# Performance work log

Hardware: AMD Instinct MI355X
Metric: run time of the kernel (lower is better)

The kernel has to match this reference:

```python
import jax, jax.numpy as jnp
import numpy as np

L_COMPUTE = 32   # topological levels after primary inputs
W = 32768        # gates per level
K = 4            # max fan-in (distinct pins 1..K per gate)
B = 128          # parallel test patterns
T = 16           # number of cell types in the library
N = (L_COMPUTE + 1) * W


def setup_inputs() -> dict:
    key = jax.random.key(0)
    k1, k2, k3, k4 = jax.random.split(key, 4)
    # binary logic values per node per pattern (only level-0 rows are real inputs;
    # the rest are overwritten by propagation, matching g.ndata['h'] = feature)
    feature = jax.random.bernoulli(k1, 0.5, (N, B)).astype(jnp.float32)
    # truth table: activation[cell_type, input_combination] in {0,1}
    activation = jax.random.bernoulli(k2, 0.5, (T, 2 ** K)).astype(jnp.float32)
    # each gate in level l draws its K inputs from level l-1
    src_idx = jax.random.randint(k3, (L_COMPUTE, W, K), 0, W).astype(jnp.int32)
    cell_type = jax.random.randint(k4, (L_COMPUTE, W), 0, T).astype(jnp.int32)
    # edge pin numbers: distinct pins 1..K per gate (edges.data['x'])
    pins = jnp.broadcast_to(jnp.arange(1, K + 1, dtype=jnp.int32), (L_COMPUTE, W, K))
    pins = jnp.asarray(pins)
    return {"feature": feature, "activation": activation, "src_idx": src_idx,
            "cell_type": cell_type, "pins": pins}


def reference(feature, activation, src_idx, cell_type, pins):
    Wn = src_idx.shape[1]
    Bn = feature.shape[1]
    h0 = feature[:Wn]  # primary-input level keeps its feature values

    def step(h, xs):
        src, ctype, pin = xs          # [W,K], [W], [W,K]
        hs = h[src]                   # gather: [W,K,B]
        # gcn_msg: m = 2^(x-1) * h_src ; gcn_reduce: sum over incoming edges
        w = jnp.exp2(pin.astype(h.dtype) - 1.0)          # [W,K]
        m = jnp.einsum('wk,wkb->wb', w, hs)              # [W,B] encoded input combo
        # NodeApplyModule: truth-table lookup activation[cell_type, h]
        h_new = activation[ctype[:, None], m.astype(jnp.int32)]  # [W,B]
        return h_new, h_new

    _, ys = jax.lax.scan(step, h0, (src_idx, cell_type, pins))
    # g.ndata.pop('h'): values for ALL nodes, level 0 unchanged
    return jnp.concatenate([h0, ys.reshape(-1, Bn)], axis=0)
```

## Files before the change

### kernel.cpp

```cpp
#include <hip/hip_runtime.h>
#include <stdint.h>

typedef uint32_t u32;
typedef unsigned long long u64;
typedef float f4 __attribute__((ext_vector_type(4)));

#define WGATES 32768
#define BATCH  128
#define LAYERS 32
#define NTYPES 16
#define NC 128
#define WPL (WGATES * 4)
#define F4L (WGATES * BATCH / 4)

#define WS_SUB_OFF    1024
#define WS_LVL2_OFF   34816
#define WS_DONE_OFF   35840
#define WS_S_OFF      69632
#define WS_NEED_BYTES ((size_t)(WS_S_OFF + 33 * WPL) * 4)

__device__ __forceinline__ u32 agent_load(const u32* p) {
    return __hip_atomic_load(p, __ATOMIC_RELAXED, __HIP_MEMORY_SCOPE_AGENT);
}
__device__ __forceinline__ void agent_store(u32* p, u32 v) {
    __hip_atomic_store(p, v, __ATOMIC_RELAXED, __HIP_MEMORY_SCOPE_AGENT);
}
__device__ __forceinline__ void agent_store64(u64* p, u64 v) {
    __hip_atomic_store(p, v, __ATOMIC_RELAXED, __HIP_MEMORY_SCOPE_AGENT);
}
__device__ __forceinline__ u32 agent_add(u32* p, u32 v) {
    return __hip_atomic_fetch_add(p, v, __ATOMIC_RELAXED, __HIP_MEMORY_SCOPE_AGENT);
}

__device__ __forceinline__ void lut_masks(u32 tt, u32 m[16]) {
    #pragma unroll
    for (int j = 0; j < 16; ++j)
        m[j] = (u32)(((int)(tt << (31 - j))) >> 31);
}
__device__ __forceinline__ u32 lut_mux(const u32 m[16], u32 a, u32 b, u32 c, u32 d) {
    u32 na = ~a, nb = ~b, nc = ~c, nd = ~d;
    u32 v0 = (m[1]&a)|(m[0]&na),  v1 = (m[3]&a)|(m[2]&na);
    u32 v2 = (m[5]&a)|(m[4]&na),  v3 = (m[7]&a)|(m[6]&na);
    u32 v4 = (m[9]&a)|(m[8]&na),  v5 = (m[11]&a)|(m[10]&na);
    u32 v6 = (m[13]&a)|(m[12]&na),v7 = (m[15]&a)|(m[14]&na);
    u32 u0 = (b&v1)|(nb&v0), u1 = (b&v3)|(nb&v2);
    u32 u2 = (b&v5)|(nb&v4), u3 = (b&v7)|(nb&v6);
    u32 w0 = (c&u1)|(nc&u0), w1 = (c&u3)|(nc&u2);
    return (d&w1)|(nd&w0);
}

__device__ __forceinline__ void wait_done(const u32* ws, int l, int line,
                                          int tid, int slp) {
    if (tid == 0) {
        const u32* p = ws + WS_DONE_OFF + (size_t)l * 1024 + line * 16;
        if (slp == 1) { while (agent_load(p) == 0) __builtin_amdgcn_s_sleep(1); }
        else         { while (agent_load(p) == 0) __builtin_amdgcn_s_sleep(8); }
    }
    __syncthreads();
    asm volatile("" ::: "memory");
}

__global__ void pack_main(const float* __restrict__ feature,
                          const float* __restrict__ activation,
                          u32* __restrict__ ws) {
    int t = blockIdx.x * 256 + threadIdx.x;
    if (blockIdx.x == 0 && threadIdx.x < NTYPES) {
        u32 tt = 0;
        #pragma unroll
        for (int m = 0; m < 16; ++m)
            tt |= (activation[threadIdx.x * 16 + m] != 0.0f ? 1u : 0u) << m;
        ws[threadIdx.x] = tt;
    }
    int z = (int)blockIdx.x - 1;
    if (z >= 0 && z < 268)
        ws[1024 + z * 256 + threadIdx.x] = 0;
    float v = feature[t];
    u64 m = __ballot(v != 0.0f);
    if ((t & 63) == 0)
        ((u64*)(ws + WS_S_OFF))[t >> 6] = m;
}

__global__ __launch_bounds__(256) void coop_kernel(
        const int* __restrict__ src_idx,
        const int* __restrict__ cell_type,
        u32* __restrict__ ws,
        float* __restrict__ out,
        int NU)
{
    u32* Sb = ws + WS_S_OFF;
    int tid = threadIdx.x;
    __shared__ u32 stt[NTYPES];
    if (tid < NTYPES) stt[tid] = ws[tid];
    __syncthreads();

    if ((int)blockIdx.x < NC) {
        int g = blockIdx.x * 256 + tid;
        int sub = blockIdx.x & 15;
        for (int l = 1; l <= LAYERS; ++l) {
            const int4 s = ((const int4*)(src_idx + (size_t)(l - 1) * WGATES * 4))[g];
            u32 ttv = stt[cell_type[(size_t)(l - 1) * WGATES + g]];
            if (l > 1) wait_done(ws, l - 1, sub, tid, 1);
            const uint4* Sp = (const uint4*)(Sb + (size_t)(l - 1) * WPL);
            uint4 A = Sp[(u32)s.x];
            uint4 B = Sp[(u32)s.y];
            uint4 C = Sp[(u32)s.z];
            uint4 D = Sp[(u32)s.w];
            u32 m[16];
            lut_masks(ttv, m);
            u32 r0 = lut_mux(m, A.x, B.x, C.x, D.x);
            u32 r1 = lut_mux(m, A.y, B.y, C.y, D.y);
            u32 r2 = lut_mux(m, A.z, B.z, C.z, D.z);
            u32 r3 = lut_mux(m, A.w, B.w, C.w, D.w);
            u64* dst = (u64*)(Sb + (size_t)l * WPL + (size_t)g * 4);
            agent_store64(dst,     ((u64)r1 << 32) | r0);
            agent_store64(dst + 1, ((u64)r3 << 32) | r2);
            asm volatile("s_waitcnt vmcnt(0)" ::: "memory");
            __syncthreads();
            if (tid == 0) {
                u32* subp = ws + WS_SUB_OFF + (size_t)l * 1024 + sub * 16;
                u32 old = agent_add(subp, 1u);
                if (old == (u32)(NC / 16 - 1)) {
                    u32 old2 = agent_add(ws + WS_LVL2_OFF + (size_t)l * 16, 1u);
                    if (old2 == 15u) {
                        u32* donep = ws + WS_DONE_OFF + (size_t)l * 1024;
                        #pragma unroll
                        for (int j = 0; j < 64; ++j)
                            agent_store(donep + j * 16, 1u);
                    }
                }
            }
        }
    } else {
        int ub = blockIdx.x - NC;
        bool sliced = (NU & 7) == 0;
        int x = ub & 7;
        u32 per = (u32)(NU >> 3);
        for (int l = 0; l <= LAYERS; ++l) {
            if (l >= 1) wait_done(ws, l, ub & 63, tid, 8);
            const u32* Sl = Sb + (size_t)l * WPL;
            f4* ob = (f4*)(out + (size_t)l * WGATES * BATCH);
            if (sliced) {
                u32 sbeg = (u32)x * (F4L / 8), send = sbeg + F4L / 8;
                for (u32 i = sbeg + (u32)(ub >> 3) * 256u + tid; i < send;
                     i += per * 256u) {
                    u32 wb = Sl[i >> 3];
                    u32 sh = (i & 7) * 4;
                    f4 f;
                    f.x = ((wb >> (sh    )) & 1) ? 1.0f : 0.0f;
                    f.y = ((wb >> (sh + 1)) & 1) ? 1.0f : 0.0f;
                    f.z = ((wb >> (sh + 2)) & 1) ? 1.0f : 0.0f;
                    f.w = ((wb >> (sh + 3)) & 1) ? 1.0f : 0.0f;
                    __builtin_nontemporal_store(f, ob + i);
                }
            } else {
                for (u32 i = (u32)ub * 256u + tid; i < (u32)F4L;
                     i += (u32)NU * 256u) {
                    u32 wb = Sl[i >> 3];
                    u32 sh = (i & 7) * 4;
                    f4 f;
                    f.x = ((wb >> (sh    )) & 1) ? 1.0f : 0.0f;
                    f.y = ((wb >> (sh + 1)) & 1) ? 1.0f : 0.0f;
                    f.z = ((wb >> (sh + 2)) & 1) ? 1.0f : 0.0f;
                    f.w = ((wb >> (sh + 3)) & 1) ? 1.0f : 0.0f;
                    __builtin_nontemporal_store(f, ob + i);
                }
            }
        }
    }
}

__global__ void pack_kernel_fb(const float* __restrict__ feature,
                               const float* __restrict__ activation,
                               float* __restrict__ out,
                               u32* __restrict__ tt_ws,
                               u32* __restrict__ buf0) {
    int t = blockIdx.x * 256 + threadIdx.x;
    if (blockIdx.x == 0 && threadIdx.x < NTYPES) {
        u32 tt = 0;
        #pragma unroll
        for (int m = 0; m < 16; ++m)
            tt |= (activation[threadIdx.x * 16 + m] != 0.0f ? 1u : 0u) << m;
        tt_ws[threadIdx.x] = tt;
    }
    float v = feature[t];
    out[t] = v;
    u64 m = __ballot(v != 0.0f);
    if ((t & 63) == 0)
        ((u64*)buf0)[t >> 6] = m;
}

__global__ void fused_kernel_fb(const u32* __restrict__ prev,
                                u32* __restrict__ next,
                                const int* __restrict__ src_idx,
                                const int* __restrict__ cell_type,
                                const u32* __restrict__ tt_ws,
                                const u32* __restrict__ upacked,
                                float* __restrict__ uout,
                                int do_compute)
{
    int tid = threadIdx.x;
    if (do_compute && blockIdx.x < 512) {
        int gl = tid >> 2, q = tid & 3;
        int wg = blockIdx.x * 64 + gl;
        const int4 s = ((const int4*)src_idx)[wg];
        u32 tt = tt_ws[cell_type[wg]];
        u32 m[16];
        lut_masks(tt, m);
        u32 a = prev[(size_t)s.x * 4 + q];
        u32 b = prev[(size_t)s.y * 4 + q];
        u32 c = prev[(size_t)s.z * 4 + q];
        u32 d = prev[(size_t)s.w * 4 + q];
        next[(size_t)wg * 4 + q] = lut_mux(m, a, b, c, d);
        return;
    }
    if (uout == nullptr) return;
    int ub = do_compute ? (int)blockIdx.x - 512 : (int)blockIdx.x;
    #pragma unroll
    for (int r = 0; r < 2; ++r) {
        int fi = ((ub * 2 + r) * 256 + tid) * 4;
        u32 wb = upacked[fi >> 5];
        int sh = fi & 31;
        f4 f;
        f.x = ((wb >> (sh    )) & 1) ? 1.0f : 0.0f;
        f.y = ((wb >> (sh + 1)) & 1) ? 1.0f : 0.0f;
        f.z = ((wb >> (sh + 2)) & 1) ? 1.0f : 0.0f;
        f.w = ((wb >> (sh + 3)) & 1) ? 1.0f : 0.0f;
        ((f4*)uout)[fi >> 2] = f;
    }
}

static void launch_fallback(const float* feature, const float* activation,
                            const int* src_idx, const int* cell_type,
                            float* out, void* d_ws, hipStream_t stream) {
    u32* tt_ws = (u32*)d_ws;
    u32* bufA = (u32*)((char*)d_ws + 1024);
    u32* bufB = (u32*)((char*)d_ws + 1024 + WGATES * 16);
    pack_kernel_fb<<<WGATES * BATCH / 256, 256, 0, stream>>>(
        feature, activation, out, tt_ws, bufA);
    for (int l = 1; l <= LAYERS; ++l) {
        u32* prev = ((l - 1) & 1) ? bufB : bufA;
        u32* next = ((l - 1) & 1) ? bufA : bufB;
        float* uout = (l >= 2) ? out + (size_t)(l - 1) * WGATES * BATCH : nullptr;
        fused_kernel_fb<<<512 + 2048, 256, 0, stream>>>(
            prev, next,
            src_idx + (size_t)(l - 1) * WGATES * 4,
            cell_type + (size_t)(l - 1) * WGATES,
            tt_ws, prev, uout, 1);
    }
    u32* s32 = ((LAYERS - 1) & 1) ? bufA : bufB;
    fused_kernel_fb<<<2048, 256, 0, stream>>>(
        s32, s32, src_idx, cell_type, tt_ws,
        s32, out + (size_t)LAYERS * WGATES * BATCH, 0);
}

extern "C" void kernel_launch(void* const* d_in, const int* in_sizes, int n_in,
                              void* d_out, int out_size, void* d_ws, size_t ws_size,
                              hipStream_t stream) {
    const float* feature    = (const float*)d_in[0];
    const float* activation = (const float*)d_in[1];
    const int*   src_idx    = (const int*)d_in[2];
    const int*   cell_type  = (const int*)d_in[3];
    float* out = (float*)d_out;

    bool coop_ok = (ws_size >= WS_NEED_BYTES);
    int G = 0, NU = 0;
    if (coop_ok) {
        int dev = 0;
        (void)hipGetDevice(&dev);
        int numCU = 0, bpc = 0;
        if (hipDeviceGetAttribute(&numCU, hipDeviceAttributeMultiprocessorCount, dev)
                != hipSuccess) coop_ok = false;
        if (coop_ok &&
            hipOccupancyMaxActiveBlocksPerMultiprocessor(
                &bpc, (const void*)coop_kernel, 256, 0) != hipSuccess) coop_ok = false;
        if (coop_ok) {
            G = bpc * numCU;
            if (G > 2048) G = 2048;
            NU = G - NC;
            if (NU < 256) coop_ok = false;
        }
    }

    if (coop_ok) {
        u32* ws = (u32*)d_ws;
        pack_main<<<WGATES * BATCH / 256, 256, 0, stream>>>(feature, activation, ws);
        void* args[] = {(void*)&src_idx, (void*)&cell_type, (void*)&ws,
                        (void*)&out, (void*)&NU};
        hipError_t e = hipLaunchCooperativeKernel(
            (const void*)coop_kernel, dim3(G), dim3(256), args, 0, stream);
        if (e == hipSuccess) return;
    }
    launch_fallback(feature, activation, src_idx, cell_type, out, d_ws, stream);
}
```

Before: 166.6 us.

## Compute two levels per grid barrier by recomputing level-1 fan-in gates redundantly

Each compute block now handles two topological levels per barrier round. For the second level it recomputes its four first-level input gates directly from the level l-2 state, so grid-wide barriers drop from 32 to 16. The price is about 5x more gathers and LUT evaluations per round and a larger register footprint. The writer blocks now wait per round and emit two levels at a time.

```diff
diff --git a/kernel.cpp b/kernel.cpp
--- a/kernel.cpp
+++ b/kernel.cpp
@@ -8,6 +8,7 @@
 #define WGATES 32768
 #define BATCH  128
 #define LAYERS 32
+#define NROUND (LAYERS / 2)
 #define NTYPES 16
 #define NC 128
 #define WPL (WGATES * 4)
@@ -49,10 +50,10 @@
     return (d&w1)|(nd&w0);
 }
 
-__device__ __forceinline__ void wait_done(const u32* ws, int l, int line,
+__device__ __forceinline__ void wait_done(const u32* ws, int r, int line,
                                           int tid, int slp) {
     if (tid == 0) {
-        const u32* p = ws + WS_DONE_OFF + (size_t)l * 1024 + line * 16;
+        const u32* p = ws + WS_DONE_OFF + (size_t)r * 1024 + line * 16;
         if (slp == 1) { while (agent_load(p) == 0) __builtin_amdgcn_s_sleep(1); }
         else         { while (agent_load(p) == 0) __builtin_amdgcn_s_sleep(8); }
     }
@@ -96,33 +97,75 @@
     if ((int)blockIdx.x < NC) {
         int g = blockIdx.x * 256 + tid;
         int sub = blockIdx.x & 15;
-        for (int l = 1; l <= LAYERS; ++l) {
-            const int4 s = ((const int4*)(src_idx + (size_t)(l - 1) * WGATES * 4))[g];
-            u32 ttv = stt[cell_type[(size_t)(l - 1) * WGATES + g]];
-            if (l > 1) wait_done(ws, l - 1, sub, tid, 1);
-            const uint4* Sp = (const uint4*)(Sb + (size_t)(l - 1) * WPL);
-            uint4 A = Sp[(u32)s.x];
-            uint4 B = Sp[(u32)s.y];
-            uint4 C = Sp[(u32)s.z];
-            uint4 D = Sp[(u32)s.w];
+        for (int r = 1; r <= NROUND; ++r) {
+            const int l1 = 2 * r - 1, l2 = 2 * r;
+            const int4* S1 = (const int4*)(src_idx + (size_t)(l1 - 1) * WGATES * 4);
+            const int4* S2 = (const int4*)(src_idx + (size_t)(l2 - 1) * WGATES * 4);
+            const int*  C1 = cell_type + (size_t)(l1 - 1) * WGATES;
+            const int*  C2 = cell_type + (size_t)(l2 - 1) * WGATES;
+            int4 i1 = S1[g];
+            int4 i2 = S2[g];
+            u32 c1 = stt[C1[g]];
+            u32 c2 = stt[C2[g]];
+            int4 j0 = S1[(u32)i2.x];  u32 cj0 = stt[C1[i2.x]];
+            int4 j1 = S1[(u32)i2.y];  u32 cj1 = stt[C1[i2.y]];
+            int4 j2 = S1[(u32)i2.z];  u32 cj2 = stt[C1[i2.z]];
+            int4 j3 = S1[(u32)i2.w];  u32 cj3 = stt[C1[i2.w]];
+
+            if (r > 1) wait_done(ws, r - 1, sub, tid, 1);
+
+            const uint4* Sp = (const uint4*)(Sb + (size_t)(2 * r - 2) * WPL);
+            uint4 A  = Sp[(u32)i1.x], B  = Sp[(u32)i1.y],
+                  C  = Sp[(u32)i1.z], D  = Sp[(u32)i1.w];
+            uint4 A0 = Sp[(u32)j0.x], B0 = Sp[(u32)j0.y],
+                  C0 = Sp[(u32)j0.z], D0 = Sp[(u32)j0.w];
+            uint4 A1 = Sp[(u32)j1.x], B1 = Sp[(u32)j1.y],
+                  C1v= Sp[(u32)j1.z], D1 = Sp[(u32)j1.w];
+            uint4 A2 = Sp[(u32)j2.x], B2 = Sp[(u32)j2.y],
+                  C2v= Sp[(u32)j2.z], D2 = Sp[(u32)j2.w];
+            uint4 A3 = Sp[(u32)j3.x], B3 = Sp[(u32)j3.y],
+                  C3 = Sp[(u32)j3.z], D3 = Sp[(u32)j3.w];
+
             u32 m[16];
-            lut_masks(ttv, m);
-            u32 r0 = lut_mux(m, A.x, B.x, C.x, D.x);
-            u32 r1 = lut_mux(m, A.y, B.y, C.y, D.y);
-            u32 r2 = lut_mux(m, A.z, B.z, C.z, D.z);
-            u32 r3 = lut_mux(m, A.w, B.w, C.w, D.w);
-            u64* dst = (u64*)(Sb + (size_t)l * WPL + (size_t)g * 4);
-            agent_store64(dst,     ((u64)r1 << 32) | r0);
-            agent_store64(dst + 1, ((u64)r3 << 32) | r2);
+            lut_masks(c1, m);
+            u32 o0 = lut_mux(m, A.x, B.x, C.x, D.x);
+            u32 o1 = lut_mux(m, A.y, B.y, C.y, D.y);
+            u32 o2 = lut_mux(m, A.z, B.z, C.z, D.z);
+            u32 o3 = lut_mux(m, A.w, B.w, C.w, D.w);
+            u64* d1 = (u64*)(Sb + (size_t)l1 * WPL + (size_t)g * 4);
+            agent_store64(d1,     ((u64)o1 << 32) | o0);
+            agent_store64(d1 + 1, ((u64)o3 << 32) | o2);
+            uint4 s0, s1v, s2v, s3v;
+            lut_masks(cj0, m);
+            s0.x = lut_mux(m, A0.x,B0.x,C0.x,D0.x); s0.y = lut_mux(m, A0.y,B0.y,C0.y,D0.y);
+            s0.z = lut_mux(m, A0.z,B0.z,C0.z,D0.z); s0.w = lut_mux(m, A0.w,B0.w,C0.w,D0.w);
+            lut_masks(cj1, m);
+            s1v.x = lut_mux(m, A1.x,B1.x,C1v.x,D1.x); s1v.y = lut_mux(m, A1.y,B1.y,C1v.y,D1.y);
+            s1v.z = lut_mux(m, A1.z,B1.z,C1v.z,D1.z); s1v.w = lut_mux(m, A1.w,B1.w,C1v.w,D1.w);
+            lut_masks(cj2, m);
+            s2v.x = lut_mux(m, A2.x,B2.x,C2v.x,D2.x); s2v.y = lut_mux(m, A2.y,B2.y,C2v.y,D2.y);
+            s2v.z = lut_mux(m, A2.z,B2.z,C2v.z,D2.z); s2v.w = lut_mux(m, A2.w,B2.w,C2v.w,D2.w);
+            lut_masks(cj3, m);
+            s3v.x = lut_mux(m, A3.x,B3.x,C3.x,D3.x); s3v.y = lut_mux(m, A3.y,B3.y,C3.y,D3.y);
+            s3v.z = lut_mux(m, A3.z,B3.z,C3.z,D3.z); s3v.w = lut_mux(m, A3.w,B3.w,C3.w,D3.w);
+            lut_masks(c2, m);
+            u32 e0 = lut_mux(m, s0.x, s1v.x, s2v.x, s3v.x);
+            u32 e1 = lut_mux(m, s0.y, s1v.y, s2v.y, s3v.y);
+            u32 e2 = lut_mux(m, s0.z, s1v.z, s2v.z, s3v.z);
+            u32 e3 = lut_mux(m, s0.w, s1v.w, s2v.w, s3v.w);
+            u64* d2 = (u64*)(Sb + (size_t)l2 * WPL + (size_t)g * 4);
+            agent_store64(d2,     ((u64)e1 << 32) | e0);
+            agent_store64(d2 + 1, ((u64)e3 << 32) | e2);
+
             asm volatile("s_waitcnt vmcnt(0)" ::: "memory");
             __syncthreads();
             if (tid == 0) {
-                u32* subp = ws + WS_SUB_OFF + (size_t)l * 1024 + sub * 16;
+                u32* subp = ws + WS_SUB_OFF + (size_t)r * 1024 + sub * 16;
                 u32 old = agent_add(subp, 1u);
                 if (old == (u32)(NC / 16 - 1)) {
-                    u32 old2 = agent_add(ws + WS_LVL2_OFF + (size_t)l * 16, 1u);
+                    u32 old2 = agent_add(ws + WS_LVL2_OFF + (size_t)r * 16, 1u);
                     if (old2 == 15u) {
-                        u32* donep = ws + WS_DONE_OFF + (size_t)l * 1024;
+                        u32* donep = ws + WS_DONE_OFF + (size_t)r * 1024;
                         #pragma unroll
                         for (int j = 0; j < 64; ++j)
                             agent_store(donep + j * 16, 1u);
@@ -135,34 +178,38 @@
         bool sliced = (NU & 7) == 0;
         int x = ub & 7;
         u32 per = (u32)(NU >> 3);
-        for (int l = 0; l <= LAYERS; ++l) {
-            if (l >= 1) wait_done(ws, l, ub & 63, tid, 8);
-            const u32* Sl = Sb + (size_t)l * WPL;
-            f4* ob = (f4*)(out + (size_t)l * WGATES * BATCH);
-            if (sliced) {
-                u32 sbeg = (u32)x * (F4L / 8), send = sbeg + F4L / 8;
-                for (u32 i = sbeg + (u32)(ub >> 3) * 256u + tid; i < send;
-                     i += per * 256u) {
-                    u32 wb = Sl[i >> 3];
-                    u32 sh = (i & 7) * 4;
-                    f4 f;
-                    f.x = ((wb >> (sh    )) & 1) ? 1.0f : 0.0f;
-                    f.y = ((wb >> (sh + 1)) & 1) ? 1.0f : 0.0f;
-                    f.z = ((wb >> (sh + 2)) & 1) ? 1.0f : 0.0f;
-                    f.w = ((wb >> (sh + 3)) & 1) ? 1.0f : 0.0f;
-                    __builtin_nontemporal_store(f, ob + i);
-                }
-            } else {
-                for (u32 i = (u32)ub * 256u + tid; i < (u32)F4L;
-                     i += (u32)NU * 256u) {
-                    u32 wb = Sl[i >> 3];
-                    u32 sh = (i & 7) * 4;
-                    f4 f;
-                    f.x = ((wb >> (sh    )) & 1) ? 1.0f : 0.0f;
-                    f.y = ((wb >> (sh + 1)) & 1) ? 1.0f : 0.0f;
-                    f.z = ((wb >> (sh + 2)) & 1) ? 1.0f : 0.0f;
-                    f.w = ((wb >> (sh + 3)) & 1) ? 1.0f : 0.0f;
-                    __builtin_nontemporal_store(f, ob + i);
+        for (int r = 0; r <= NROUND; ++r) {
+            if (r >= 1) wait_done(ws, r, ub & 63, tid, 8);
+            int lbeg = (r == 0) ? 0 : 2 * r - 1;
+            int lend = (r == 0) ? 0 : 2 * r;
+            for (int l = lbeg; l <= lend; ++l) {
+                const u32* Sl = Sb + (size_t)l * WPL;
+                f4* ob = (f4*)(out + (size_t)l * WGATES * BATCH);
+                if (sliced) {
+                    u32 sbeg = (u32)x * (F4L / 8), send = sbeg + F4L / 8;
+                    for (u32 i = sbeg + (u32)(ub >> 3) * 256u + tid; i < send;
+                         i += per * 256u) {
+                        u32 wb = Sl[i >> 3];
+                        u32 sh = (i & 7) * 4;
+                        f4 f;
+                        f.x = ((wb >> (sh    )) & 1) ? 1.0f : 0.0f;
+                        f.y = ((wb >> (sh + 1)) & 1) ? 1.0f : 0.0f;
+                        f.z = ((wb >> (sh + 2)) & 1) ? 1.0f : 0.0f;
+                        f.w = ((wb >> (sh + 3)) & 1) ? 1.0f : 0.0f;
+                        __builtin_nontemporal_store(f, ob + i);
+                    }
+                } else {
+                    for (u32 i = (u32)ub * 256u + tid; i < (u32)F4L;
+                         i += (u32)NU * 256u) {
+                        u32 wb = Sl[i >> 3];
+                        u32 sh = (i & 7) * 4;
+                        f4 f;
+                        f.x = ((wb >> (sh    )) & 1) ? 1.0f : 0.0f;
+                        f.y = ((wb >> (sh + 1)) & 1) ? 1.0f : 0.0f;
+                        f.z = ((wb >> (sh + 2)) & 1) ? 1.0f : 0.0f;
+                        f.w = ((wb >> (sh + 3)) & 1) ? 1.0f : 0.0f;
+                        __builtin_nontemporal_store(f, ob + i);
+                    }
                 }
             }
         }
```

Result: slower. 249.5 us (+49.8%).

## Replace per-level barrier with epoch-tagged words for dataflow synchronization

Applied to the files above, without the earlier changes.

Adds a coop_epoch kernel that stores each packed 32-bit word next to a 32-bit level tag. Compute blocks now gather their inputs optimistically and spin only on entries whose tag is stale, instead of waiting on a full level barrier. The barrier signal is deferred and used only by the unpacking blocks, and next-level indices are prefetched early. This doubles the workspace footprint and the gather bytes, and it relies on relaxed 64-bit atomic visibility. The path is selected only when the workspace is large enough, otherwise the old kernel runs.

```diff
diff --git a/kernel.cpp b/kernel.cpp
--- a/kernel.cpp
+++ b/kernel.cpp
@@ -17,13 +17,17 @@
 #define WS_LVL2_OFF   34816
 #define WS_DONE_OFF   35840
 #define WS_S_OFF      69632
-#define WS_NEED_BYTES ((size_t)(WS_S_OFF + 33 * WPL) * 4)
+#define WS_NEED_V8    ((size_t)(WS_S_OFF + 33 * WPL) * 4)
+#define WS_NEED_EP    ((size_t)WS_S_OFF * 4 + (size_t)33 * WPL * 8)
 
 __device__ __forceinline__ u32 agent_load(const u32* p) {
     return __hip_atomic_load(p, __ATOMIC_RELAXED, __HIP_MEMORY_SCOPE_AGENT);
 }
 __device__ __forceinline__ void agent_store(u32* p, u32 v) {
     __hip_atomic_store(p, v, __ATOMIC_RELAXED, __HIP_MEMORY_SCOPE_AGENT);
+}
+__device__ __forceinline__ u64 agent_load64(const u64* p) {
+    return __hip_atomic_load(p, __ATOMIC_RELAXED, __HIP_MEMORY_SCOPE_AGENT);
 }
 __device__ __forceinline__ void agent_store64(u64* p, u64 v) {
     __hip_atomic_store(p, v, __ATOMIC_RELAXED, __HIP_MEMORY_SCOPE_AGENT);
@@ -62,7 +66,7 @@
 
 __global__ void pack_main(const float* __restrict__ feature,
                           const float* __restrict__ activation,
-                          u32* __restrict__ ws) {
+                          u32* __restrict__ ws, int tagged) {
     int t = blockIdx.x * 256 + threadIdx.x;
     if (blockIdx.x == 0 && threadIdx.x < NTYPES) {
         u32 tt = 0;
@@ -76,11 +80,147 @@
         ws[1024 + z * 256 + threadIdx.x] = 0;
     float v = feature[t];
     u64 m = __ballot(v != 0.0f);
-    if ((t & 63) == 0)
-        ((u64*)(ws + WS_S_OFF))[t >> 6] = m;
-}
-
-__global__ __launch_bounds__(256) void coop_kernel(
+    if ((t & 63) == 0) {
+        u32 k = (u32)(t >> 6);
+        if (tagged) {
+            u64* S0 = (u64*)(ws + WS_S_OFF);
+            S0[2 * k]     = (u64)(u32)m;
+            S0[2 * k + 1] = (m >> 32);
+        } else {
+            ((u64*)(ws + WS_S_OFF))[k] = m;
+        }
+    }
+}
+
+#define FIXQ(X, P)                                                          \
+    while ((X).y != expt || (X).w != expt) {                                \
+        u64 fa = agent_load64(P); u64 fb = agent_load64((P) + 1);           \
+        (X).x = (u32)fa; (X).y = (u32)(fa >> 32);                           \
+        (X).z = (u32)fb; (X).w = (u32)(fb >> 32);                           \
+        if ((X).y == expt && (X).w == expt) break;                          \
+        __builtin_amdgcn_s_sleep(1);                                        \
+    }
+
+__global__ __launch_bounds__(256) void coop_epoch(
+        const int* __restrict__ src_idx,
+        const int* __restrict__ cell_type,
+        u32* __restrict__ ws,
+        float* __restrict__ out,
+        int NU)
+{
+    u64* S64 = (u64*)(ws + WS_S_OFF);
+    int tid = threadIdx.x;
+    __shared__ u32 stt[NTYPES];
+    if (tid < NTYPES) stt[tid] = ws[tid];
+    __syncthreads();
+
+    if ((int)blockIdx.x < NC) {
+        int g = blockIdx.x * 256 + tid;
+        int sub = blockIdx.x & 15;
+        const int4* SI = (const int4*)src_idx;
+        int4 idx = SI[g];
+        int ctv = cell_type[g];
+        for (int l = 1; l <= LAYERS; ++l) {
+            const u64* Sp = S64 + (size_t)(l - 1) * WPL;
+            u64* Sn = S64 + (size_t)l * WPL;
+            u32 expt = (u32)(l - 1);
+            const u64* pa = Sp + (size_t)(u32)idx.x * 4;
+            const u64* pb = Sp + (size_t)(u32)idx.y * 4;
+            const u64* pc = Sp + (size_t)(u32)idx.z * 4;
+            const u64* pd = Sp + (size_t)(u32)idx.w * 4;
+            uint4 A0 = *(const uint4*)pa, A1 = *(const uint4*)(pa + 2);
+            uint4 B0 = *(const uint4*)pb, B1 = *(const uint4*)(pb + 2);
+            uint4 C0 = *(const uint4*)pc, C1 = *(const uint4*)(pc + 2);
+            uint4 D0 = *(const uint4*)pd, D1 = *(const uint4*)(pd + 2);
+            int4 idxn = idx; int ctn = ctv;
+            if (l < LAYERS) {
+                idxn = SI[(size_t)l * WGATES + g];
+                ctn = cell_type[(size_t)l * WGATES + g];
+            }
+            if (l > 1) {
+                asm volatile("s_waitcnt vmcnt(0)" ::: "memory");
+                __syncthreads();
+                if (tid == 0) {
+                    u32* subp = ws + WS_SUB_OFF + (size_t)(l - 1) * 1024 + sub * 16;
+                    if (agent_add(subp, 1u) == (u32)(NC / 16 - 1)) {
+                        if (agent_add(ws + WS_LVL2_OFF + (size_t)(l - 1) * 16, 1u) == 15u) {
+                            u32* donep = ws + WS_DONE_OFF + (size_t)(l - 1) * 1024;
+                            #pragma unroll
+                            for (int j = 0; j < 64; ++j)
+                                agent_store(donep + j * 16, 1u);
+                        }
+                    }
+                }
+            }
+            FIXQ(A0, pa) FIXQ(A1, pa + 2)
+            FIXQ(B0, pb) FIXQ(B1, pb + 2)
+            FIXQ(C0, pc) FIXQ(C1, pc + 2)
+            FIXQ(D0, pd) FIXQ(D1, pd + 2)
+            u32 m[16];
+            lut_masks(stt[ctv], m);
+            u32 r0 = lut_mux(m, A0.x, B0.x, C0.x, D0.x);
+            u32 r1 = lut_mux(m, A0.z, B0.z, C0.z, D0.z);
+            u32 r2 = lut_mux(m, A1.x, B1.x, C1.x, D1.x);
+            u32 r3 = lut_mux(m, A1.z, B1.z, C1.z, D1.z);
+            u64* dst = Sn + (size_t)g * 4;
+            u64 tg = (u64)(u32)l << 32;
+            agent_store64(dst + 0, tg | r0);
+            agent_store64(dst + 1, tg | r1);
+            agent_store64(dst + 2, tg | r2);
+            agent_store64(dst + 3, tg | r3);
+            idx = idxn; ctv = ctn;
+        }
+        asm volatile("s_waitcnt vmcnt(0)" ::: "memory");
+        __syncthreads();
+        if (tid == 0) {
+            u32* subp = ws + WS_SUB_OFF + (size_t)LAYERS * 1024 + sub * 16;
+            if (agent_add(subp, 1u) == (u32)(NC / 16 - 1)) {
+                if (agent_add(ws + WS_LVL2_OFF + (size_t)LAYERS * 16, 1u) == 15u) {
+                    u32* donep = ws + WS_DONE_OFF + (size_t)LAYERS * 1024;
+                    #pragma unroll
+                    for (int j = 0; j < 64; ++j)
+                        agent_store(donep + j * 16, 1u);
+                }
+            }
+        }
+    } else {
+        int ub = blockIdx.x - NC;
+        bool sliced = (NU & 7) == 0;
+        int x = ub & 7;
+        u32 per = (u32)(NU >> 3);
+        for (int l = 0; l <= LAYERS; ++l) {
+            if (l >= 1) wait_done(ws, l, ub & 63, tid, 8);
+            const u64* Sl = S64 + (size_t)l * WPL;
+            u32 expt = (u32)l;
+            f4* ob = (f4*)(out + (size_t)l * WGATES * BATCH);
+            u32 ibeg, iend, istep;
+            if (sliced) {
+                ibeg = (u32)x * (F4L / 8) + (u32)(ub >> 3) * 256u + tid;
+                iend = (u32)x * (F4L / 8) + F4L / 8;
+                istep = per * 256u;
+            } else {
+                ibeg = (u32)ub * 256u + tid; iend = (u32)F4L; istep = (u32)NU * 256u;
+            }
+            for (u32 i = ibeg; i < iend; i += istep) {
+                u64 v = Sl[i >> 3];
+                if ((u32)(v >> 32) != expt) {
+                    do { v = agent_load64(Sl + (i >> 3)); }
+                    while ((u32)(v >> 32) != expt);
+                }
+                u32 wb = (u32)v;
+                u32 sh = (i & 7) * 4;
+                f4 f;
+                f.x = ((wb >> (sh    )) & 1) ? 1.0f : 0.0f;
+                f.y = ((wb >> (sh + 1)) & 1) ? 1.0f : 0.0f;
+                f.z = ((wb >> (sh + 2)) & 1) ? 1.0f : 0.0f;
+                f.w = ((wb >> (sh + 3)) & 1) ? 1.0f : 0.0f;
+                __builtin_nontemporal_store(f, ob + i);
+            }
+        }
+    }
+}
+
+__global__ __launch_bounds__(256) void coop_v8(
         const int* __restrict__ src_idx,
         const int* __restrict__ cell_type,
         u32* __restrict__ ws,
@@ -118,10 +258,8 @@
             __syncthreads();
             if (tid == 0) {
                 u32* subp = ws + WS_SUB_OFF + (size_t)l * 1024 + sub * 16;
-                u32 old = agent_add(subp, 1u);
-                if (old == (u32)(NC / 16 - 1)) {
-                    u32 old2 = agent_add(ws + WS_LVL2_OFF + (size_t)l * 16, 1u);
-                    if (old2 == 15u) {
+                if (agent_add(subp, 1u) == (u32)(NC / 16 - 1)) {
+                    if (agent_add(ws + WS_LVL2_OFF + (size_t)l * 16, 1u) == 15u) {
                         u32* donep = ws + WS_DONE_OFF + (size_t)l * 1024;
                         #pragma unroll
                         for (int j = 0; j < 64; ++j)
@@ -139,31 +277,23 @@
             if (l >= 1) wait_done(ws, l, ub & 63, tid, 8);
             const u32* Sl = Sb + (size_t)l * WPL;
             f4* ob = (f4*)(out + (size_t)l * WGATES * BATCH);
+            u32 ibeg, iend, istep;
             if (sliced) {
-                u32 sbeg = (u32)x * (F4L / 8), send = sbeg + F4L / 8;
-                for (u32 i = sbeg + (u32)(ub >> 3) * 256u + tid; i < send;
-                     i += per * 256u) {
-                    u32 wb = Sl[i >> 3];
-                    u32 sh = (i & 7) * 4;
-                    f4 f;
-                    f.x = ((wb >> (sh    )) & 1) ? 1.0f : 0.0f;
-                    f.y = ((wb >> (sh + 1)) & 1) ? 1.0f : 0.0f;
-                    f.z = ((wb >> (sh + 2)) & 1) ? 1.0f : 0.0f;
-                    f.w = ((wb >> (sh + 3)) & 1) ? 1.0f : 0.0f;
-                    __builtin_nontemporal_store(f, ob + i);
-                }
+                ibeg = (u32)x * (F4L / 8) + (u32)(ub >> 3) * 256u + tid;
+                iend = (u32)x * (F4L / 8) + F4L / 8;
+                istep = per * 256u;
             } else {
-                for (u32 i = (u32)ub * 256u + tid; i < (u32)F4L;
-                     i += (u32)NU * 256u) {
-                    u32 wb = Sl[i >> 3];
-                    u32 sh = (i & 7) * 4;
-                    f4 f;
-                    f.x = ((wb >> (sh    )) & 1) ? 1.0f : 0.0f;
-                    f.y = ((wb >> (sh + 1)) & 1) ? 1.0f : 0.0f;
-                    f.z = ((wb >> (sh + 2)) & 1) ? 1.0f : 0.0f;
-                    f.w = ((wb >> (sh + 3)) & 1) ? 1.0f : 0.0f;
-                    __builtin_nontemporal_store(f, ob + i);
-                }
+                ibeg = (u32)ub * 256u + tid; iend = (u32)F4L; istep = (u32)NU * 256u;
+            }
+            for (u32 i = ibeg; i < iend; i += istep) {
+                u32 wb = Sl[i >> 3];
+                u32 sh = (i & 7) * 4;
+                f4 f;
+                f.x = ((wb >> (sh    )) & 1) ? 1.0f : 0.0f;
+                f.y = ((wb >> (sh + 1)) & 1) ? 1.0f : 0.0f;
+                f.z = ((wb >> (sh + 2)) & 1) ? 1.0f : 0.0f;
+                f.w = ((wb >> (sh + 3)) & 1) ? 1.0f : 0.0f;
+                __builtin_nontemporal_store(f, ob + i);
             }
         }
     }
@@ -262,8 +392,11 @@
     const int*   cell_type  = (const int*)d_in[3];
     float* out = (float*)d_out;
 
-    bool coop_ok = (ws_size >= WS_NEED_BYTES);
+    bool use_ep = (ws_size >= WS_NEED_EP);
+    bool use_v8 = !use_ep && (ws_size >= WS_NEED_V8);
     int G = 0, NU = 0;
+    bool coop_ok = use_ep || use_v8;
+    const void* kfn = use_ep ? (const void*)coop_epoch : (const void*)coop_v8;
     if (coop_ok) {
         int dev = 0;
         (void)hipGetDevice(&dev);
@@ -272,7 +405,7 @@
                 != hipSuccess) coop_ok = false;
         if (coop_ok &&
             hipOccupancyMaxActiveBlocksPerMultiprocessor(
-                &bpc, (const void*)coop_kernel, 256, 0) != hipSuccess) coop_ok = false;
+                &bpc, kfn, 256, 0) != hipSuccess) coop_ok = false;
         if (coop_ok) {
             G = bpc * numCU;
             if (G > 2048) G = 2048;
@@ -283,11 +416,13 @@
 
     if (coop_ok) {
         u32* ws = (u32*)d_ws;
-        pack_main<<<WGATES * BATCH / 256, 256, 0, stream>>>(feature, activation, ws);
+        int tagged = use_ep ? 1 : 0;
+        pack_main<<<WGATES * BATCH / 256, 256, 0, stream>>>(
+            feature, activation, ws, tagged);
         void* args[] = {(void*)&src_idx, (void*)&cell_type, (void*)&ws,
                         (void*)&out, (void*)&NU};
         hipError_t e = hipLaunchCooperativeKernel(
-            (const void*)coop_kernel, dim3(G), dim3(256), args, 0, stream);
+            kfn, dim3(G), dim3(256), args, 0, stream);
         if (e == hipSuccess) return;
     }
     launch_fallback(feature, activation, src_idx, cell_type, out, d_ws, stream);
```

Result: slower. 235.5 us (+41.4%).
